# Performance work log

Hardware: AMD Instinct MI355X
Metric: run time of the kernel (lower is better)

Reference implementation:

```python
import jax, jax.numpy as jnp
import numpy as np
from jax.scipy.special import logsumexp

T, B, N = 512, 512, 64  # time, batch, labels


def setup_inputs() -> dict:
    key = jax.random.key(0)
    k1, k2, k3, k4, k5, k6 = jax.random.split(key, 6)
    scale = 1.0 / np.sqrt(N).astype(np.float32)  # matches init.normal_(0, 1/sqrt(N))
    emit = jax.random.normal(k1, (T, B, N), jnp.float32)
    transitions = jax.random.normal(k2, (N, N), jnp.float32) * scale
    strans = jax.random.normal(k3, (N,), jnp.float32) * scale
    etrans = jax.random.normal(k4, (N,), jnp.float32) * scale
    target = jax.random.randint(k5, (T, B), 0, N)
    lengths = jax.random.randint(k6, (B,), 1, T + 1)  # at least 1 valid step
    mask = jnp.arange(T)[:, None] < lengths[None, :]  # (T, B) bool, mask[0] all True
    return {"emit": emit, "transitions": transitions, "strans": strans,
            "etrans": etrans, "target": target, "mask": mask}


def reference(emit, transitions, strans, etrans, target, mask):
    # ---- get_logZ: semiring (logsumexp) scan over time ----
    def step(alpha, xs):
        emit_i, mask_i = xs  # (B, N), (B,)
        # scores[b, j] = logsumexp_i alpha[b, i] + trans[i, j] + emit_i[b, j]
        scores = logsumexp(alpha[:, :, None] + transitions[None, :, :]
                           + emit_i[:, None, :], axis=1)
        alpha = jnp.where(mask_i[:, None], scores, alpha)
        return alpha, None

    alpha0 = emit[0] + strans  # (B, N)
    alpha, _ = jax.lax.scan(step, alpha0, (emit[1:], mask[1:]))
    logZ = logsumexp(alpha + etrans, axis=1).sum()

    # ---- score: gold-path score ----
    trans_sc = transitions[target[:-1], target[1:]]                 # (T-1, B)
    emit_sc = jnp.take_along_axis(emit, target[:, :, None], axis=2)[..., 0]  # (T, B)
    step_sc = emit_sc.at[1:].add(trans_sc)
    gold = jnp.where(mask, step_sc, 0.0).sum()
    ends = mask.sum(axis=0) - 1                                     # (B,) last valid step
    gold = gold + strans[target[0]].sum()
    gold = gold + etrans[target[ends, jnp.arange(B)]].sum()

    # negative log-likelihood (standard CRF loss = logZ - gold score)
    return logZ - gold
```

## Files before the change

kernel.cpp:

```cpp
#include <hip/hip_runtime.h>

#define TT 512
#define BB 512
#define NN 64
#define LN2F 0.69314718055994530942f
#define SCH 64
#define EXACT_THRESH 32

typedef _Float16 half8_t __attribute__((ext_vector_type(8)));
typedef float    f32x4   __attribute__((ext_vector_type(4)));

union AFrag { int u[4]; half8_t h; };

__device__ __forceinline__ float wave_max(float v) {
    #pragma unroll
    for (int off = 32; off > 0; off >>= 1)
        v = fmaxf(v, __shfl_xor(v, off, 64));
    return v;
}

__device__ __forceinline__ float wave_sum(float v) {
    #pragma unroll
    for (int off = 32; off > 0; off >>= 1)
        v += __shfl_xor(v, off, 64);
    return v;
}

__device__ __forceinline__ int wave_sum_i(int v) {
    #pragma unroll
    for (int off = 32; off > 0; off >>= 1)
        v += __shfl_xor(v, off, 64);
    return v;
}

__device__ __forceinline__ float bcast_lane(float v, int lane) {
    return __uint_as_float(__builtin_amdgcn_readlane(__float_as_uint(v), lane));
}

__global__ void zero_kernel(float* __restrict__ out) {
    if (threadIdx.x == 0 && blockIdx.x == 0) out[0] = 0.0f;
}

__global__ __launch_bounds__(576) void crf_fwd_kernel(
    const float* __restrict__ emit,
    const float* __restrict__ trans,
    const float* __restrict__ strans,
    const float* __restrict__ etrans,
    const int*   __restrict__ target,
    const void*  __restrict__ maskp,
    float* __restrict__ out)
{
    const int b   = blockIdx.x;
    const int tid = threadIdx.x;
    const int k   = tid & 63;
    const int wv  = tid >> 6;

    __shared__ float FL[8][NN];
    __shared__ float RL[8][NN];
    __shared__ int   EFs[8], ERs[8];

    const int*           mi32 = (const int*)maskp;
    const unsigned char* mi8  = (const unsigned char*)maskp;
    const bool bytemode = (mi32[0] == 0x01010101);

    int cnt = 0;
    #pragma unroll
    for (int i = 0; i < TT / 64; ++i) {
        const size_t tb = (size_t)(i * 64 + k) * BB + b;
        cnt += bytemode ? (mi8[tb] != 0) : (mi32[tb] != 0);
    }
    const int len = wave_sum_i(cnt);

    const int  q    = k >> 4;
    const int  nlo  = k & 15;
    const bool bit4 = (k & 16) != 0;
    const bool bit5 = (k & 32) != 0;

    const float* eptr = emit + (size_t)b * NN + k;

    int addrs[8];
    #pragma unroll
    for (int kh = 0; kh < 2; ++kh)
        #pragma unroll
        for (int r = 0; r < 4; ++r)
            addrs[4 * kh + r] = 128 * kh + 32 * q + 8 * r;

    const f32x4 zero4 = {0.f, 0.f, 0.f, 0.f};

    auto ldrow = [&](int t) -> float {
        t = t < 0 ? 0 : (t >= TT ? TT - 1 : t);
        return eptr[(size_t)t * BB * NN];
    };

    half8_t BfF[4][2], BfB[4][2];
    if (wv < 8) {
        #pragma unroll
        for (int g = 0; g < 4; ++g) {
            #pragma unroll
            for (int kh = 0; kh < 2; ++kh) {
                AFrag bf, bb;
                #pragma unroll
                for (int jp = 0; jp < 4; ++jp) {
                    const int krow = 32 * kh + 8 * q + 2 * jp;
                    const int ncol = 16 * g + nlo;
                    const float f0 = 0.25f * __expf(trans[(krow + 0) * NN + ncol]);
                    const float f1 = 0.25f * __expf(trans[(krow + 1) * NN + ncol]);
                    bf.u[jp] = __builtin_bit_cast(int, __builtin_amdgcn_cvt_pkrtz(f0, f1));
                    const float g0 = 0.25f * __expf(trans[ncol * NN + (krow + 0)]);
                    const float g1 = 0.25f * __expf(trans[ncol * NN + (krow + 1)]);
                    bb.u[jp] = __builtin_bit_cast(int, __builtin_amdgcn_cvt_pkrtz(g0, g1));
                }
                BfF[g][kh] = bf.h;
                BfB[g][kh] = bb.h;
            }
        }
    }

    auto matvec = [&](float x, const half8_t Bf[4][2]) -> float {
        const float uo = __int_as_float(
            __builtin_amdgcn_mov_dpp(__float_as_int(x), 0xB1, 0xF, 0xF, true));
        const int pkv = __builtin_bit_cast(int, __builtin_amdgcn_cvt_pkrtz(x, uo));
        AFrag a0f, a1f;
        #pragma unroll
        for (int r = 0; r < 4; ++r) {
            a0f.u[r] = __builtin_amdgcn_ds_bpermute(addrs[r],     pkv);
            a1f.u[r] = __builtin_amdgcn_ds_bpermute(addrs[4 + r], pkv);
        }
        const f32x4 aA0 = __builtin_amdgcn_mfma_f32_16x16x32_f16(a0f.h, Bf[0][0], zero4, 0, 0, 0);
        const f32x4 aA1 = __builtin_amdgcn_mfma_f32_16x16x32_f16(a0f.h, Bf[1][0], zero4, 0, 0, 0);
        const f32x4 aA2 = __builtin_amdgcn_mfma_f32_16x16x32_f16(a0f.h, Bf[2][0], zero4, 0, 0, 0);
        const f32x4 aA3 = __builtin_amdgcn_mfma_f32_16x16x32_f16(a0f.h, Bf[3][0], zero4, 0, 0, 0);
        const f32x4 ac0 = __builtin_amdgcn_mfma_f32_16x16x32_f16(a1f.h, Bf[0][1], aA0, 0, 0, 0);
        const f32x4 ac1 = __builtin_amdgcn_mfma_f32_16x16x32_f16(a1f.h, Bf[1][1], aA1, 0, 0, 0);
        const f32x4 ac2 = __builtin_amdgcn_mfma_f32_16x16x32_f16(a1f.h, Bf[2][1], aA2, 0, 0, 0);
        const f32x4 ac3 = __builtin_amdgcn_mfma_f32_16x16x32_f16(a1f.h, Bf[3][1], aA3, 0, 0, 0);
        const float sLo = bit4 ? ac1[0] : ac0[0];
        const float sHi = bit4 ? ac3[0] : ac2[0];
        return bit5 ? sHi : sLo;
    };

    float uF = 1.f, uB = 1.f;
    int   eF = 0,  eB = 0;
    float m0 = 0.f;

    auto stepF = [&](float w) {
        const float yown = matvec(uF, BfF);
        const int e = (int)((__builtin_amdgcn_readfirstlane(__float_as_uint(yown)) >> 23) & 0xff) - 127 + 4;
        uF = ldexpf(yown * w, -e);
        eF += e + 2;
    };
    auto stepB = [&](float w) {
        const float yown = matvec(uB * w, BfB);
        const int e = (int)((__builtin_amdgcn_readfirstlane(__float_as_uint(yown)) >> 23) & 0xff) - 127 + 4;
        uB = ldexpf(yown, -e);
        eB += e + 2;
    };

    if (wv < 8) {
        const int t0  = 1 + SCH * wv;
        const int nst = max(0, min(len - t0, SCH));
        const bool dob = (wv > 0);

        if (wv == 0) {
            const float alpha0 = eptr[0] + strans[k];
            m0 = bcast_lane(alpha0, 0);
            uF = __expf(alpha0 - m0);
        }

        const int tL = t0 + nst - 1;
        float fa = ldrow(t0 + 0), fb = ldrow(t0 + 1), fc = ldrow(t0 + 2), fd = ldrow(t0 + 3);
        float ba = ldrow(tL - 0), bbv = ldrow(tL - 1), bcv = ldrow(tL - 2), bdv = ldrow(tL - 3);
        int i = 0;
        for (; i + 4 <= nst; i += 4) {
            const float wf0 = __expf(fa), wf1 = __expf(fb), wf2 = __expf(fc), wf3 = __expf(fd);
            const float wb0 = __expf(ba), wb1 = __expf(bbv), wb2 = __expf(bcv), wb3 = __expf(bdv);
            fa  = ldrow(t0 + i + 4); fb  = ldrow(t0 + i + 5); fc  = ldrow(t0 + i + 6); fd  = ldrow(t0 + i + 7);
            ba  = ldrow(tL - i - 4); bbv = ldrow(tL - i - 5); bcv = ldrow(tL - i - 6); bdv = ldrow(tL - i - 7);
            stepF(wf0); if (dob) stepB(wb0);
            stepF(wf1); if (dob) stepB(wb1);
            stepF(wf2); if (dob) stepB(wb2);
            stepF(wf3); if (dob) stepB(wb3);
        }
        if (i     < nst) { stepF(__expf(fa)); if (dob) stepB(__expf(ba));  }
        if (i + 1 < nst) { stepF(__expf(fb)); if (dob) stepB(__expf(bbv)); }
        if (i + 2 < nst) { stepF(__expf(fc)); if (dob) stepB(__expf(bcv)); }

        FL[wv][k] = uF;
        RL[wv][k] = uB;
        if (k == 0) { EFs[wv] = eF; ERs[wv] = eB; }
    } else {
        int tvals[TT / 64];
        #pragma unroll
        for (int i = 0; i < TT / 64; ++i)
            tvals[i] = target[(size_t)(64 * i + k) * BB + b];

        float g = 0.f;
        int prev_last = 0;
        #pragma unroll
        for (int i = 0; i < TT / 64; ++i) {
            const int tt = 64 * i + k;
            const int tgt = tvals[i];
            int tprev = __shfl_up(tvals[i], 1, 64);
            if (k == 0) tprev = prev_last;
            prev_last = __builtin_amdgcn_readlane(tvals[i], 63);
            if (tt < len) {
                float v = emit[((size_t)tt * BB + b) * NN + tgt];
                v += (tt == 0) ? strans[tgt] : trans[tprev * NN + tgt];
                if (tt == len - 1) v += etrans[tgt];
                g += v;
            }
        }
        g = wave_sum(g);
        if (k == 0) atomicAdd(out, -g);
    }

    __syncthreads();

    if (wv == 0) {
        float Ltot = LN2F * (float)EFs[0];
        float x = FL[0][k];

        const int  Bc  = (len >= 2) ? ((len - 2) / SCH) : 0;
        const int  tB0 = 1 + SCH * Bc;
        const int  sB  = len - tB0;
        const bool exact = (Bc >= 1) && (sB < EXACT_THRESH);
        const int  Cend  = exact ? Bc - 1 : Bc;

        for (int c = 1; c <= Cend; ++c) {
            const float num = wave_sum(RL[c][k] * x);
            const float den = wave_sum(FL[c][k]);
            Ltot += __logf(num / den) + LN2F * (float)ERs[c];
            x = FL[c][k];
        }

        if (exact) {
            uF = x; eF = 0;
            float pa = ldrow(tB0 + 0), pb = ldrow(tB0 + 1), pc = ldrow(tB0 + 2), pd = ldrow(tB0 + 3);
            int i = 0;
            for (; i + 4 <= sB; i += 4) {
                const float w0 = __expf(pa), w1 = __expf(pb), w2 = __expf(pc), w3 = __expf(pd);
                pa = ldrow(tB0 + i + 4); pb = ldrow(tB0 + i + 5);
                pc = ldrow(tB0 + i + 6); pd = ldrow(tB0 + i + 7);
                stepF(w0); stepF(w1); stepF(w2); stepF(w3);
            }
            if (i     < sB) stepF(__expf(pa));
            if (i + 1 < sB) stepF(__expf(pb));
            if (i + 2 < sB) stepF(__expf(pc));
            x = uF;
            Ltot += LN2F * (float)eF;
        }

        const float la = __logf(x) + etrans[k];
        const float m2 = wave_max(la);
        const float sm = wave_sum(__expf(la - m2));
        const float logZ_b = m0 + Ltot + m2 + __logf(sm);

        if (k == 0) atomicAdd(out, logZ_b);
    }
}

extern "C" void kernel_launch(void* const* d_in, const int* in_sizes, int n_in,
                              void* d_out, int out_size, void* d_ws, size_t ws_size,
                              hipStream_t stream) {
    const float* emit   = (const float*)d_in[0];
    const float* trans  = (const float*)d_in[1];
    const float* strans = (const float*)d_in[2];
    const float* etrans = (const float*)d_in[3];
    const int*   target = (const int*)d_in[4];
    const void*  mask   = d_in[5];
    float* out = (float*)d_out;

    hipLaunchKernelGGL(zero_kernel, dim3(1), dim3(64), 0, stream, out);
    hipLaunchKernelGGL(crf_fwd_kernel, dim3(BB), dim3(576), 0, stream,
                       emit, trans, strans, etrans, target, mask, out);
}
```

Baseline: 168.7 us.

## Split forward and backward chunk scans onto separate waves in 16-wave blocks

Each wave now runs either a forward or a backward chunk scan instead of interleaving both on one wave. Block size grows from 9 to 16 waves (15 scan waves plus the gold-score wave) and each wave holds only one set of B fragments. The gold score is passed through shared memory and folded into a single atomic per block. This shortens the serial dependency chain per wave to one matvec per step, at the cost of larger blocks and possibly lower residency per CU.

New measurement: 193.2 us. +14.5%, slower.

```diff
diff --git a/kernel.cpp b/kernel.cpp
--- a/kernel.cpp
+++ b/kernel.cpp
@@ -41,7 +41,7 @@
     if (threadIdx.x == 0 && blockIdx.x == 0) out[0] = 0.0f;
 }
 
-__global__ __launch_bounds__(576) void crf_fwd_kernel(
+__global__ __launch_bounds__(1024, 4) void crf_fwd_kernel(
     const float* __restrict__ emit,
     const float* __restrict__ trans,
     const float* __restrict__ strans,
@@ -57,7 +57,8 @@
 
     __shared__ float FL[8][NN];
     __shared__ float RL[8][NN];
-    __shared__ int   EFs[8], ERs[8];
+    __shared__ int   esF[8], esB[8];
+    __shared__ float gsh;
 
     const int*           mi32 = (const int*)maskp;
     const unsigned char* mi8  = (const unsigned char*)maskp;
@@ -87,36 +88,21 @@
 
     const f32x4 zero4 = {0.f, 0.f, 0.f, 0.f};
 
-    auto ldrow = [&](int t) -> float {
-        t = t < 0 ? 0 : (t >= TT ? TT - 1 : t);
+    const int  Bc    = (len >= 2) ? ((len - 2) / SCH) : 0;
+    const int  sB    = len - (1 + SCH * Bc);
+    const bool exact = (Bc >= 1) && (sB < EXACT_THRESH);
+
+    auto ldr = [&](int t) -> float {
+        t = t < 0 ? 0 : (t > TT - 1 ? TT - 1 : t);
         return eptr[(size_t)t * BB * NN];
     };
 
-    half8_t BfF[4][2], BfB[4][2];
-    if (wv < 8) {
-        #pragma unroll
-        for (int g = 0; g < 4; ++g) {
-            #pragma unroll
-            for (int kh = 0; kh < 2; ++kh) {
-                AFrag bf, bb;
-                #pragma unroll
-                for (int jp = 0; jp < 4; ++jp) {
-                    const int krow = 32 * kh + 8 * q + 2 * jp;
-                    const int ncol = 16 * g + nlo;
-                    const float f0 = 0.25f * __expf(trans[(krow + 0) * NN + ncol]);
-                    const float f1 = 0.25f * __expf(trans[(krow + 1) * NN + ncol]);
-                    bf.u[jp] = __builtin_bit_cast(int, __builtin_amdgcn_cvt_pkrtz(f0, f1));
-                    const float g0 = 0.25f * __expf(trans[ncol * NN + (krow + 0)]);
-                    const float g1 = 0.25f * __expf(trans[ncol * NN + (krow + 1)]);
-                    bb.u[jp] = __builtin_bit_cast(int, __builtin_amdgcn_cvt_pkrtz(g0, g1));
-                }
-                BfF[g][kh] = bf.h;
-                BfB[g][kh] = bb.h;
-            }
-        }
-    }
-
-    auto matvec = [&](float x, const half8_t Bf[4][2]) -> float {
+    half8_t Bf[4][2];
+    float m0loc = 0.f;
+    float uX = 1.f;
+    int   eX = 0;
+
+    auto matvec = [&](float x) -> float {
         const float uo = __int_as_float(
             __builtin_amdgcn_mov_dpp(__float_as_int(x), 0xB1, 0xF, 0xF, true));
         const int pkv = __builtin_bit_cast(int, __builtin_amdgcn_cvt_pkrtz(x, uo));
@@ -139,55 +125,74 @@
         return bit5 ? sHi : sLo;
     };
 
-    float uF = 1.f, uB = 1.f;
-    int   eF = 0,  eB = 0;
-    float m0 = 0.f;
-
     auto stepF = [&](float w) {
-        const float yown = matvec(uF, BfF);
-        const int e = (int)((__builtin_amdgcn_readfirstlane(__float_as_uint(yown)) >> 23) & 0xff) - 127 + 4;
-        uF = ldexpf(yown * w, -e);
-        eF += e + 2;
+        const float y = matvec(uX);
+        const int e = (int)((__builtin_amdgcn_readfirstlane(__float_as_uint(y)) >> 23) & 0xff) - 127 + 4;
+        uX = ldexpf(y * w, -e);
+        eX += e + 2;
     };
     auto stepB = [&](float w) {
-        const float yown = matvec(uB * w, BfB);
-        const int e = (int)((__builtin_amdgcn_readfirstlane(__float_as_uint(yown)) >> 23) & 0xff) - 127 + 4;
-        uB = ldexpf(yown, -e);
-        eB += e + 2;
-    };
-
-    if (wv < 8) {
-        const int t0  = 1 + SCH * wv;
-        const int nst = max(0, min(len - t0, SCH));
-        const bool dob = (wv > 0);
-
-        if (wv == 0) {
+        const float y = matvec(uX * w);
+        const int e = (int)((__builtin_amdgcn_readfirstlane(__float_as_uint(y)) >> 23) & 0xff) - 127 + 4;
+        uX = ldexpf(y, -e);
+        eX += e + 2;
+    };
+
+    if (wv < 15) {
+        const bool fwd = (wv < 8);
+        const int  c   = fwd ? wv : (wv - 7);
+
+        #pragma unroll
+        for (int g = 0; g < 4; ++g) {
+            #pragma unroll
+            for (int kh = 0; kh < 2; ++kh) {
+                AFrag bf;
+                #pragma unroll
+                for (int jp = 0; jp < 4; ++jp) {
+                    const int krow = 32 * kh + 8 * q + 2 * jp;
+                    const int ncol = 16 * g + nlo;
+                    float e0, e1;
+                    if (fwd) {
+                        e0 = 0.25f * __expf(trans[(krow + 0) * NN + ncol]);
+                        e1 = 0.25f * __expf(trans[(krow + 1) * NN + ncol]);
+                    } else {
+                        e0 = 0.25f * __expf(trans[ncol * NN + (krow + 0)]);
+                        e1 = 0.25f * __expf(trans[ncol * NN + (krow + 1)]);
+                    }
+                    bf.u[jp] = __builtin_bit_cast(int, __builtin_amdgcn_cvt_pkrtz(e0, e1));
+                }
+                Bf[g][kh] = bf.h;
+            }
+        }
+
+        if (fwd && c == 0) {
             const float alpha0 = eptr[0] + strans[k];
-            m0 = bcast_lane(alpha0, 0);
-            uF = __expf(alpha0 - m0);
-        }
-
-        const int tL = t0 + nst - 1;
-        float fa = ldrow(t0 + 0), fb = ldrow(t0 + 1), fc = ldrow(t0 + 2), fd = ldrow(t0 + 3);
-        float ba = ldrow(tL - 0), bbv = ldrow(tL - 1), bcv = ldrow(tL - 2), bdv = ldrow(tL - 3);
+            m0loc = bcast_lane(alpha0, 0);
+            uX = __expf(alpha0 - m0loc);
+        }
+
+        const int t0  = 1 + SCH * c;
+        const int nst = min(max(len - t0, 0), SCH);
+        const int tL  = t0 + nst - 1;
+
+        auto rowd = [&](int j) -> float { return ldr(fwd ? (t0 + j) : (tL - j)); };
+
+        float r0 = rowd(0), r1 = rowd(1), r2 = rowd(2), r3 = rowd(3);
         int i = 0;
+        #pragma unroll 1
         for (; i + 4 <= nst; i += 4) {
-            const float wf0 = __expf(fa), wf1 = __expf(fb), wf2 = __expf(fc), wf3 = __expf(fd);
-            const float wb0 = __expf(ba), wb1 = __expf(bbv), wb2 = __expf(bcv), wb3 = __expf(bdv);
-            fa  = ldrow(t0 + i + 4); fb  = ldrow(t0 + i + 5); fc  = ldrow(t0 + i + 6); fd  = ldrow(t0 + i + 7);
-            ba  = ldrow(tL - i - 4); bbv = ldrow(tL - i - 5); bcv = ldrow(tL - i - 6); bdv = ldrow(tL - i - 7);
-            stepF(wf0); if (dob) stepB(wb0);
-            stepF(wf1); if (dob) stepB(wb1);
-            stepF(wf2); if (dob) stepB(wb2);
-            stepF(wf3); if (dob) stepB(wb3);
-        }
-        if (i     < nst) { stepF(__expf(fa)); if (dob) stepB(__expf(ba));  }
-        if (i + 1 < nst) { stepF(__expf(fb)); if (dob) stepB(__expf(bbv)); }
-        if (i + 2 < nst) { stepF(__expf(fc)); if (dob) stepB(__expf(bcv)); }
-
-        FL[wv][k] = uF;
-        RL[wv][k] = uB;
-        if (k == 0) { EFs[wv] = eF; ERs[wv] = eB; }
+            const float w0 = __expf(r0), w1 = __expf(r1);
+            const float w2 = __expf(r2), w3 = __expf(r3);
+            r0 = rowd(i + 4); r1 = rowd(i + 5); r2 = rowd(i + 6); r3 = rowd(i + 7);
+            if (fwd) { stepF(w0); stepF(w1); stepF(w2); stepF(w3); }
+            else     { stepB(w0); stepB(w1); stepB(w2); stepB(w3); }
+        }
+        if (i     < nst) { const float w = __expf(r0); fwd ? stepF(w) : stepB(w); }
+        if (i + 1 < nst) { const float w = __expf(r1); fwd ? stepF(w) : stepB(w); }
+        if (i + 2 < nst) { const float w = __expf(r2); fwd ? stepF(w) : stepB(w); }
+
+        if (fwd) { FL[c][k] = uX; if (k == 0) esF[c] = eX; }
+        else     { RL[c][k] = uX; if (k == 0) esB[c] = eX; }
     } else {
         int tvals[TT / 64];
         #pragma unroll
@@ -211,51 +216,50 @@
             }
         }
         g = wave_sum(g);
-        if (k == 0) atomicAdd(out, -g);
+        if (k == 0) gsh = g;
     }
 
     __syncthreads();
 
     if (wv == 0) {
-        float Ltot = LN2F * (float)EFs[0];
-        float x = FL[0][k];
-
-        const int  Bc  = (len >= 2) ? ((len - 2) / SCH) : 0;
-        const int  tB0 = 1 + SCH * Bc;
-        const int  sB  = len - tB0;
-        const bool exact = (Bc >= 1) && (sB < EXACT_THRESH);
-        const int  Cend  = exact ? Bc - 1 : Bc;
-
-        for (int c = 1; c <= Cend; ++c) {
-            const float num = wave_sum(RL[c][k] * x);
-            const float den = wave_sum(FL[c][k]);
-            Ltot += __logf(num / den) + LN2F * (float)ERs[c];
-            x = FL[c][k];
+        float x    = FL[0][k];
+        float Ltot = LN2F * (float)esF[0];
+        const int Cend = exact ? (Bc - 1) : Bc;
+
+        for (int c2 = 1; c2 <= Cend; ++c2) {
+            const float num = wave_sum(RL[c2][k] * x);
+            const float den = wave_sum(FL[c2][k]);
+            Ltot += __logf(num / den) + LN2F * (float)esB[c2];
+            x = FL[c2][k];
         }
 
         if (exact) {
-            uF = x; eF = 0;
-            float pa = ldrow(tB0 + 0), pb = ldrow(tB0 + 1), pc = ldrow(tB0 + 2), pd = ldrow(tB0 + 3);
-            int i = 0;
-            for (; i + 4 <= sB; i += 4) {
-                const float w0 = __expf(pa), w1 = __expf(pb), w2 = __expf(pc), w3 = __expf(pd);
-                pa = ldrow(tB0 + i + 4); pb = ldrow(tB0 + i + 5);
-                pc = ldrow(tB0 + i + 6); pd = ldrow(tB0 + i + 7);
+            uX = x; eX = 0;
+            const int t0B = 1 + SCH * Bc;
+            float p0 = ldr(t0B + 0), p1 = ldr(t0B + 1);
+            float p2 = ldr(t0B + 2), p3 = ldr(t0B + 3);
+            int j = 0;
+            #pragma unroll 1
+            for (; j + 4 <= sB; j += 4) {
+                const float w0 = __expf(p0), w1 = __expf(p1);
+                const float w2 = __expf(p2), w3 = __expf(p3);
+                p0 = ldr(t0B + j + 4); p1 = ldr(t0B + j + 5);
+                p2 = ldr(t0B + j + 6); p3 = ldr(t0B + j + 7);
                 stepF(w0); stepF(w1); stepF(w2); stepF(w3);
             }
-            if (i     < sB) stepF(__expf(pa));
-            if (i + 1 < sB) stepF(__expf(pb));
-            if (i + 2 < sB) stepF(__expf(pc));
-            x = uF;
-            Ltot += LN2F * (float)eF;
+            if (j     < sB) stepF(__expf(p0));
+            if (j + 1 < sB) stepF(__expf(p1));
+            if (j + 2 < sB) stepF(__expf(p2));
+            x = uX;
+            Ltot += LN2F * (float)eX;
         }
 
         const float la = __logf(x) + etrans[k];
         const float m2 = wave_max(la);
         const float sm = wave_sum(__expf(la - m2));
-        const float logZ_b = m0 + Ltot + m2 + __logf(sm);
-
-        if (k == 0) atomicAdd(out, logZ_b);
+        const float logZ_b = m0loc + Ltot + m2 + __logf(sm);
+
+        if (k == 0) atomicAdd(out, logZ_b - gsh);
     }
 }
 
@@ -271,6 +275,6 @@
     float* out = (float*)d_out;
 
     hipLaunchKernelGGL(zero_kernel, dim3(1), dim3(64), 0, stream, out);
-    hipLaunchKernelGGL(crf_fwd_kernel, dim3(BB), dim3(576), 0, stream,
+    hipLaunchKernelGGL(crf_fwd_kernel, dim3(BB), dim3(1024), 0, stream,
                        emit, trans, strans, etrans, target, mask, out);
 }
```
